# Kernel tuning notes

Hardware: AMD Instinct MI355X
Metric: run time of the kernel (lower is better)

The kernel has to match this reference:

```python
import jax, jax.numpy as jnp
import numpy as np


def _expm_batch(S):
    # S: [..., m, m] skew-symmetric -> elementwise matrix exponential
    flat = S.reshape((-1,) + S.shape[-2:])
    E = jax.vmap(jax.scipy.linalg.expm)(flat)
    return E.reshape(S.shape)


def _time_prod(M):
    # M: [B, T, m, m] -> Z = M[:,T-1] @ ... @ M[:,0]  (dyadic, log-depth, matches DevNet dyadic_prod order)
    B, T, m, _ = M.shape
    eye = jnp.eye(m, dtype=M.dtype)
    while M.shape[1] > 1:
        if M.shape[1] % 2 == 1:
            pad = jnp.broadcast_to(eye, (B, 1, m, m))
            M = jnp.concatenate([M, pad], axis=1)
        # later factor on the left: M[:,1::2] @ M[:,0::2]
        M = jnp.einsum('btij,btjk->btik', M[:, 1::2], M[:, 0::2])
    return M[:, 0]


def setup_inputs() -> dict:
    key = jax.random.key(0)
    k1, k2, k3 = jax.random.split(key, 3)
    B, T, Cin, m, O = 64, 2048, 8, 16, 10
    X = jax.random.normal(k1, (B, T, Cin), dtype=jnp.float32)
    A = jax.random.normal(k2, (m, m, Cin), dtype=jnp.float32) * 0.2
    W = jax.random.normal(k3, (O, m * m), dtype=jnp.float32) * (1.0 / np.sqrt(m * m))
    b = jnp.zeros((O,), dtype=jnp.float32)
    return {"X": X, "A": A, "W": W, "b": b}


def reference(X, A, W, b):
    # skew-symmetric parametrization of the Lie algebra so(m)
    A_skew = A - jnp.swapaxes(A, 0, 1)          # [m, m, Cin]
    dX = X[:, 1:] - X[:, :-1]                    # [B, T-1, Cin] path increments
    S = jnp.einsum('btc,ijc->btij', dX, A_skew)  # [B, T-1, m, m] skew per step
    M = _expm_batch(S)                           # per-step SO(m) elements
    Z = _time_prod(M)                            # [B, m, m] path development
    out = Z.reshape(Z.shape[0], -1) @ W.T + b    # [B, n_outputs]
    return out
```

## Files before the change

kernel.cpp:

```cpp
#include <hip/hip_runtime.h>

#define BSZ   64
#define TLEN  2048
#define NSTEP 2047
#define CIN   8
#define NCH   128
#define CHL   16
#define TSTR  20

typedef __attribute__((ext_vector_type(4))) float    fx4;
typedef __attribute__((ext_vector_type(4))) _Float16 hx4;

__device__ __forceinline__ void splitf(const fx4 v, hx4& hi, hx4& lo) {
    _Float16 h0 = (_Float16)v[0], h1 = (_Float16)v[1];
    _Float16 h2 = (_Float16)v[2], h3 = (_Float16)v[3];
    hi[0] = h0; hi[1] = h1; hi[2] = h2; hi[3] = h3;
    lo[0] = (_Float16)(v[0] - (float)h0);
    lo[1] = (_Float16)(v[1] - (float)h1);
    lo[2] = (_Float16)(v[2] - (float)h2);
    lo[3] = (_Float16)(v[3] - (float)h3);
}

__device__ __forceinline__ fx4 mm3(hx4 ah, hx4 al, hx4 bh, hx4 bl) {
    fx4 acc = {0.f, 0.f, 0.f, 0.f};
    acc = __builtin_amdgcn_mfma_f32_16x16x16f16(ah, bh, acc, 0, 0, 0);
    acc = __builtin_amdgcn_mfma_f32_16x16x16f16(ah, bl, acc, 0, 0, 0);
    acc = __builtin_amdgcn_mfma_f32_16x16x16f16(al, bh, acc, 0, 0, 0);
    return acc;
}

__device__ __forceinline__ fx4 ldsT(float (*ts)[TSTR], int m, int c, fx4 v) {
    ts[4 * m + 0][c] = v[0];
    ts[4 * m + 1][c] = v[1];
    ts[4 * m + 2][c] = v[2];
    ts[4 * m + 3][c] = v[3];
    return *(const fx4*)&ts[c][4 * m];
}

__global__ __launch_bounds__(256)
void devnet_expm_chunk(const float* __restrict__ X, const float* __restrict__ A,
                       float* __restrict__ G)
{
    __shared__ __align__(16) float Ts[4][16][TSTR];

    const int tid  = threadIdx.x;
    const int wid  = tid >> 6;
    const int lane = tid & 63;
    const int m    = lane >> 4;
    const int c    = lane & 15;
    const int gw   = blockIdx.x * 4 + wid;
    const int b    = gw >> 7;
    const int ch   = gw & (NCH - 1);
    float (*ts)[TSTR] = Ts[wid];

    float ask[4][CIN];
#pragma unroll
    for (int r = 0; r < 4; ++r) {
        const int i = 4 * m + r;
#pragma unroll
        for (int cc = 0; cc < CIN; ++cc)
            ask[r][cc] = A[(i * 16 + c) * CIN + cc] - A[(c * 16 + i) * CIN + cc];
    }

    fx4 idv;
#pragma unroll
    for (int r = 0; r < 4; ++r) idv[r] = (4 * m + r == c) ? 1.f : 0.f;

    fx4 P = idv;

    const int t0 = ch * CHL;
    const int t1 = (t0 + CHL < NSTEP) ? (t0 + CHL) : NSTEP;

    for (int t = t0; t < t1; ++t) {
        const float* xp = X + ((size_t)b * TLEN + t) * CIN;
        const float4 x0 = *reinterpret_cast<const float4*>(xp + 0);
        const float4 x1 = *reinterpret_cast<const float4*>(xp + 4);
        const float4 y0 = *reinterpret_cast<const float4*>(xp + 8);
        const float4 y1 = *reinterpret_cast<const float4*>(xp + 12);
        float dx[CIN];
        dx[0] = y0.x - x0.x; dx[1] = y0.y - x0.y; dx[2] = y0.z - x0.z; dx[3] = y0.w - x0.w;
        dx[4] = y1.x - x1.x; dx[5] = y1.y - x1.y; dx[6] = y1.z - x1.z; dx[7] = y1.w - x1.w;

        fx4 sv;
#pragma unroll
        for (int r = 0; r < 4; ++r) {
            float acc = 0.f;
#pragma unroll
            for (int cc = 0; cc < CIN; ++cc) acc = fmaf(dx[cc], ask[r][cc], acc);
            sv[r] = acc;
        }

        float a = fabsf(sv[0]) + fabsf(sv[1]) + fabsf(sv[2]) + fabsf(sv[3]);
        a += __shfl_xor(a, 16, 64);
        a += __shfl_xor(a, 32, 64);
        a = fmaxf(a, __shfl_xor(a, 1, 64));
        a = fmaxf(a, __shfl_xor(a, 2, 64));
        a = fmaxf(a, __shfl_xor(a, 4, 64));
        a = fmaxf(a, __shfl_xor(a, 8, 64));

        int sc = 0;
        float scale = 1.f;
        while (a > 0.5f && sc < 40) { a *= 0.5f; scale *= 0.5f; ++sc; }

        fx4 xv = sv * scale;
        fx4 nxv = -xv;
        hx4 Xah, Xal;
        splitf(nxv, Xah, Xal);

        fx4 R = idv + xv * 0.125f;
#pragma unroll
        for (int k = 7; k >= 1; --k) {
            hx4 Rh, Rl;
            splitf(R, Rh, Rl);
            fx4 acc = mm3(Xah, Xal, Rh, Rl);
            R = idv + acc * (1.f / (float)k);
        }

        for (int q = 0; q < sc; ++q) {
            fx4 Ra = ldsT(ts, m, c, R);
            hx4 Ah, Al, Bh, Bl;
            splitf(Ra, Ah, Al);
            splitf(R, Bh, Bl);
            R = mm3(Ah, Al, Bh, Bl);
        }

        {
            fx4 Ra = ldsT(ts, m, c, R);
            hx4 Ah, Al, Ph, Pl;
            splitf(Ra, Ah, Al);
            splitf(P, Ph, Pl);
            P = mm3(Ah, Al, Ph, Pl);
        }
    }

    *reinterpret_cast<fx4*>(G + ((size_t)b * NCH + ch) * 256 + lane * 4) = P;
}

__global__ __launch_bounds__(256)
void devnet_reduce(const float* __restrict__ G, const float* __restrict__ W,
                   const float* __restrict__ bias, float* __restrict__ out)
{
    __shared__ __align__(16) float Ts[4][16][TSTR];
    __shared__ __align__(16) float Fs[4][256];
    __shared__ float Zf[256];
    __shared__ float red[10][4];

    const int tid  = threadIdx.x;
    const int wid  = tid >> 6;
    const int lane = tid & 63;
    const int m    = lane >> 4;
    const int c    = lane & 15;
    const int b    = blockIdx.x;
    float (*ts)[TSTR] = Ts[wid];

    const float* gb = G + (size_t)b * NCH * 256;

    fx4 Acc = *reinterpret_cast<const fx4*>(gb + (size_t)(wid * 32) * 256 + lane * 4);
    for (int cc = 1; cc < 32; ++cc) {
        fx4 Q = *reinterpret_cast<const fx4*>(gb + (size_t)(wid * 32 + cc) * 256 + lane * 4);
        fx4 Qa = ldsT(ts, m, c, Q);
        hx4 Ah, Al, Bh, Bl;
        splitf(Qa, Ah, Al);
        splitf(Acc, Bh, Bl);
        Acc = mm3(Ah, Al, Bh, Bl);
    }
    *reinterpret_cast<fx4*>(&Fs[wid][lane * 4]) = Acc;
    __syncthreads();

    if (wid == 0) {
        for (int w2 = 1; w2 < 4; ++w2) {
            fx4 Q = *reinterpret_cast<const fx4*>(&Fs[w2][lane * 4]);
            fx4 Qa = ldsT(ts, m, c, Q);
            hx4 Ah, Al, Bh, Bl;
            splitf(Qa, Ah, Al);
            splitf(Acc, Bh, Bl);
            Acc = mm3(Ah, Al, Bh, Bl);
        }
#pragma unroll
        for (int r = 0; r < 4; ++r) Zf[(4 * m + r) * 16 + c] = Acc[r];
    }
    __syncthreads();

    const float z = Zf[tid];
    for (int o = 0; o < 10; ++o) {
        float v = z * W[o * 256 + tid];
#pragma unroll
        for (int off = 32; off >= 1; off >>= 1) v += __shfl_down(v, off, 64);
        if (lane == 0) red[o][wid] = v;
    }
    __syncthreads();
    if (tid < 10)
        out[b * 10 + tid] = red[tid][0] + red[tid][1] + red[tid][2] + red[tid][3] + bias[tid];
}

extern "C" void kernel_launch(void* const* d_in, const int* in_sizes, int n_in,
                              void* d_out, int out_size, void* d_ws, size_t ws_size,
                              hipStream_t stream)
{
    const float* X    = (const float*)d_in[0];
    const float* A    = (const float*)d_in[1];
    const float* W    = (const float*)d_in[2];
    const float* bias = (const float*)d_in[3];
    float* out = (float*)d_out;
    float* G   = (float*)d_ws;

    devnet_expm_chunk<<<BSZ * NCH / 4, 256, 0, stream>>>(X, A, G);
    devnet_reduce<<<BSZ, 256, 0, stream>>>(G, W, bias, out);
}
```

Measured before the change: 205.9 us.

## Retune expm scaling/Taylor order, pack fp16 split transpose, split reduce kernel

Computes the scaling-and-squaring exponent with frexp and scales to a smaller norm so a degree-5 Taylor series suffices instead of degree 8, cutting Horner MFMA steps at the cost of roughly one extra squaring. The squaring loop now splits R into fp16 hi/lo once and transposes packed halves through LDS, avoiding a second split. The reduction is split into two kernels with smaller blocks to spread chunk products over more CUs, adding a kernel launch. The lower Taylor order slightly changes the accuracy trade-off.

```diff
diff --git a/kernel.cpp b/kernel.cpp
--- a/kernel.cpp
+++ b/kernel.cpp
@@ -8,8 +8,10 @@
 #define CHL   16
 #define TSTR  20
 
-typedef __attribute__((ext_vector_type(4))) float    fx4;
-typedef __attribute__((ext_vector_type(4))) _Float16 hx4;
+typedef __attribute__((ext_vector_type(4))) float        fx4;
+typedef __attribute__((ext_vector_type(4))) _Float16     hx4;
+typedef __attribute__((ext_vector_type(2))) unsigned int ux2;
+typedef __attribute__((ext_vector_type(4))) unsigned int ux4;
 
 __device__ __forceinline__ void splitf(const fx4 v, hx4& hi, hx4& lo) {
     _Float16 h0 = (_Float16)v[0], h1 = (_Float16)v[1];
@@ -29,19 +31,41 @@
     return acc;
 }
 
-__device__ __forceinline__ fx4 ldsT(float (*ts)[TSTR], int m, int c, fx4 v) {
-    ts[4 * m + 0][c] = v[0];
-    ts[4 * m + 1][c] = v[1];
-    ts[4 * m + 2][c] = v[2];
-    ts[4 * m + 3][c] = v[3];
-    return *(const fx4*)&ts[c][4 * m];
+__device__ __forceinline__ fx4 ldsT(float* ts, int m, int c, fx4 v) {
+    ts[(4 * m + 0) * TSTR + c] = v[0];
+    ts[(4 * m + 1) * TSTR + c] = v[1];
+    ts[(4 * m + 2) * TSTR + c] = v[2];
+    ts[(4 * m + 3) * TSTR + c] = v[3];
+    return *(const fx4*)&ts[c * TSTR + 4 * m];
+}
+
+__device__ __forceinline__ void ldsT_h(unsigned* tsu, int m, int c,
+                                       hx4 Bh, hx4 Bl, hx4& Ah, hx4& Al) {
+    ux2 bh = __builtin_bit_cast(ux2, Bh);
+    ux2 bl = __builtin_bit_cast(ux2, Bl);
+    unsigned w0 = (bh[0] & 0xFFFFu) | (bl[0] << 16);
+    unsigned w1 = (bh[0] >> 16)     | (bl[0] & 0xFFFF0000u);
+    unsigned w2 = (bh[1] & 0xFFFFu) | (bl[1] << 16);
+    unsigned w3 = (bh[1] >> 16)     | (bl[1] & 0xFFFF0000u);
+    tsu[(4 * m + 0) * TSTR + c] = w0;
+    tsu[(4 * m + 1) * TSTR + c] = w1;
+    tsu[(4 * m + 2) * TSTR + c] = w2;
+    tsu[(4 * m + 3) * TSTR + c] = w3;
+    ux4 rd = *(const ux4*)&tsu[c * TSTR + 4 * m];
+    ux2 ah, al;
+    ah[0] = (rd[0] & 0xFFFFu) | (rd[1] << 16);
+    al[0] = (rd[0] >> 16)     | (rd[1] & 0xFFFF0000u);
+    ah[1] = (rd[2] & 0xFFFFu) | (rd[3] << 16);
+    al[1] = (rd[2] >> 16)     | (rd[3] & 0xFFFF0000u);
+    Ah = __builtin_bit_cast(hx4, ah);
+    Al = __builtin_bit_cast(hx4, al);
 }
 
 __global__ __launch_bounds__(256)
 void devnet_expm_chunk(const float* __restrict__ X, const float* __restrict__ A,
                        float* __restrict__ G)
 {
-    __shared__ __align__(16) float Ts[4][16][TSTR];
+    __shared__ __align__(16) unsigned Ts[4][16 * TSTR];
 
     const int tid  = threadIdx.x;
     const int wid  = tid >> 6;
@@ -51,7 +75,8 @@
     const int gw   = blockIdx.x * 4 + wid;
     const int b    = gw >> 7;
     const int ch   = gw & (NCH - 1);
-    float (*ts)[TSTR] = Ts[wid];
+    unsigned* tsu = Ts[wid];
+    float*    tsf = (float*)Ts[wid];
 
     float ask[4][CIN];
 #pragma unroll
@@ -98,18 +123,20 @@
         a = fmaxf(a, __shfl_xor(a, 4, 64));
         a = fmaxf(a, __shfl_xor(a, 8, 64));
 
-        int sc = 0;
-        float scale = 1.f;
-        while (a > 0.5f && sc < 40) { a *= 0.5f; scale *= 0.5f; ++sc; }
+        int e;
+        (void)frexpf(a, &e);
+        int sc = e + 2;
+        if (sc < 0) sc = 0;
+        const float scale = ldexpf(1.0f, -sc);
 
         fx4 xv = sv * scale;
         fx4 nxv = -xv;
         hx4 Xah, Xal;
         splitf(nxv, Xah, Xal);
 
-        fx4 R = idv + xv * 0.125f;
-#pragma unroll
-        for (int k = 7; k >= 1; --k) {
+        fx4 R = idv + xv * 0.2f;
+#pragma unroll
+        for (int k = 4; k >= 1; --k) {
             hx4 Rh, Rl;
             splitf(R, Rh, Rl);
             fx4 acc = mm3(Xah, Xal, Rh, Rl);
@@ -117,15 +144,14 @@
         }
 
         for (int q = 0; q < sc; ++q) {
-            fx4 Ra = ldsT(ts, m, c, R);
-            hx4 Ah, Al, Bh, Bl;
-            splitf(Ra, Ah, Al);
+            hx4 Bh, Bl, Ah, Al;
             splitf(R, Bh, Bl);
+            ldsT_h(tsu, m, c, Bh, Bl, Ah, Al);
             R = mm3(Ah, Al, Bh, Bl);
         }
 
         {
-            fx4 Ra = ldsT(ts, m, c, R);
+            fx4 Ra = ldsT(tsf, m, c, R);
             hx4 Ah, Al, Ph, Pl;
             splitf(Ra, Ah, Al);
             splitf(P, Ph, Pl);
@@ -136,61 +162,67 @@
     *reinterpret_cast<fx4*>(G + ((size_t)b * NCH + ch) * 256 + lane * 4) = P;
 }
 
-__global__ __launch_bounds__(256)
-void devnet_reduce(const float* __restrict__ G, const float* __restrict__ W,
-                   const float* __restrict__ bias, float* __restrict__ out)
-{
-    __shared__ __align__(16) float Ts[4][16][TSTR];
-    __shared__ __align__(16) float Fs[4][256];
-    __shared__ float Zf[256];
-    __shared__ float red[10][4];
-
-    const int tid  = threadIdx.x;
-    const int wid  = tid >> 6;
-    const int lane = tid & 63;
+__global__ __launch_bounds__(64)
+void devnet_reduce1(float* __restrict__ G)
+{
+    __shared__ __align__(16) float Ts[16 * TSTR];
+
+    const int lane = threadIdx.x;
     const int m    = lane >> 4;
     const int c    = lane & 15;
-    const int b    = blockIdx.x;
-    float (*ts)[TSTR] = Ts[wid];
-
-    const float* gb = G + (size_t)b * NCH * 256;
-
-    fx4 Acc = *reinterpret_cast<const fx4*>(gb + (size_t)(wid * 32) * 256 + lane * 4);
+    const int b    = blockIdx.x >> 2;
+    const int w    = blockIdx.x & 3;
+
+    float* base = G + ((size_t)b * NCH + w * 32) * 256;
+
+    fx4 Acc = *reinterpret_cast<const fx4*>(base + lane * 4);
     for (int cc = 1; cc < 32; ++cc) {
-        fx4 Q = *reinterpret_cast<const fx4*>(gb + (size_t)(wid * 32 + cc) * 256 + lane * 4);
-        fx4 Qa = ldsT(ts, m, c, Q);
+        fx4 Q  = *reinterpret_cast<const fx4*>(base + (size_t)cc * 256 + lane * 4);
+        fx4 Qa = ldsT(Ts, m, c, Q);
         hx4 Ah, Al, Bh, Bl;
         splitf(Qa, Ah, Al);
         splitf(Acc, Bh, Bl);
         Acc = mm3(Ah, Al, Bh, Bl);
     }
-    *reinterpret_cast<fx4*>(&Fs[wid][lane * 4]) = Acc;
-    __syncthreads();
-
-    if (wid == 0) {
-        for (int w2 = 1; w2 < 4; ++w2) {
-            fx4 Q = *reinterpret_cast<const fx4*>(&Fs[w2][lane * 4]);
-            fx4 Qa = ldsT(ts, m, c, Q);
-            hx4 Ah, Al, Bh, Bl;
-            splitf(Qa, Ah, Al);
-            splitf(Acc, Bh, Bl);
-            Acc = mm3(Ah, Al, Bh, Bl);
-        }
-#pragma unroll
-        for (int r = 0; r < 4; ++r) Zf[(4 * m + r) * 16 + c] = Acc[r];
-    }
-    __syncthreads();
-
-    const float z = Zf[tid];
+    *reinterpret_cast<fx4*>(base + lane * 4) = Acc;
+}
+
+__global__ __launch_bounds__(64)
+void devnet_reduce2(const float* __restrict__ G, const float* __restrict__ W,
+                    const float* __restrict__ bias, float* __restrict__ out)
+{
+    __shared__ __align__(16) float Ts[16 * TSTR];
+    __shared__ float Zf[256];
+
+    const int lane = threadIdx.x;
+    const int m    = lane >> 4;
+    const int c    = lane & 15;
+    const int b    = blockIdx.x;
+
+    const float* gb = G + (size_t)b * NCH * 256;
+
+    fx4 Acc = *reinterpret_cast<const fx4*>(gb + lane * 4);
+    for (int w = 1; w < 4; ++w) {
+        fx4 Q  = *reinterpret_cast<const fx4*>(gb + (size_t)(w * 32) * 256 + lane * 4);
+        fx4 Qa = ldsT(Ts, m, c, Q);
+        hx4 Ah, Al, Bh, Bl;
+        splitf(Qa, Ah, Al);
+        splitf(Acc, Bh, Bl);
+        Acc = mm3(Ah, Al, Bh, Bl);
+    }
+#pragma unroll
+    for (int r = 0; r < 4; ++r) Zf[(4 * m + r) * 16 + c] = Acc[r];
+
     for (int o = 0; o < 10; ++o) {
-        float v = z * W[o * 256 + tid];
+        const float* wo = W + o * 256;
+        float v = Zf[lane] * wo[lane];
+        v = fmaf(Zf[lane + 64],  wo[lane + 64],  v);
+        v = fmaf(Zf[lane + 128], wo[lane + 128], v);
+        v = fmaf(Zf[lane + 192], wo[lane + 192], v);
 #pragma unroll
         for (int off = 32; off >= 1; off >>= 1) v += __shfl_down(v, off, 64);
-        if (lane == 0) red[o][wid] = v;
-    }
-    __syncthreads();
-    if (tid < 10)
-        out[b * 10 + tid] = red[tid][0] + red[tid][1] + red[tid][2] + red[tid][3] + bias[tid];
+        if (lane == 0) out[b * 10 + o] = v + bias[o];
+    }
 }
 
 extern "C" void kernel_launch(void* const* d_in, const int* in_sizes, int n_in,
@@ -205,5 +237,6 @@
     float* G   = (float*)d_ws;
 
     devnet_expm_chunk<<<BSZ * NCH / 4, 256, 0, stream>>>(X, A, G);
-    devnet_reduce<<<BSZ, 256, 0, stream>>>(G, W, bias, out);
-}
+    devnet_reduce1<<<BSZ * 4, 64, 0, stream>>>(G);
+    devnet_reduce2<<<BSZ, 64, 0, stream>>>(G, W, bias, out);
+}
```

Result: faster. 194.5 us (-5.5%).
